# Performance work log

Measured on AMD Instinct MI355X. Metric: run time of the kernel, lower is better.

Reference implementation:

```python
import jax, jax.numpy as jnp
import numpy as np

N, E, F, R, L, B = 50000, 800000, 64, 20, 2, 64
RC = 5.0
ZMAX = 100
LN2 = 0.6931471805599453

def ssp(x):
    # shifted softplus: softplus(x) - log(2)
    return jax.nn.softplus(x) - LN2

def setup_inputs() -> dict:
    key = jax.random.key(0)
    ks = jax.random.split(key, 32)
    w = lambda i, shape: jax.random.normal(ks[i], shape, dtype=jnp.float32) * 0.05
    inp = {
        'z': jax.random.randint(ks[0], (N,), 0, ZMAX + 1),
        'pos': jax.random.normal(ks[1], (N, 3), dtype=jnp.float32) * 3.0,
        'edge_index': jax.random.randint(ks[2], (2, E), 0, N),
        'batch_idx': jnp.sort(jax.random.randint(ks[3], (N,), 0, B)),
        'emb': jax.random.normal(ks[4], (ZMAX + 1, F), dtype=jnp.float32),
        'phi_W': w(5, (L, 3 * F, F)), 'phi_b': w(6, (L, 3 * F)),
        'filt_W1': w(7, (L, F, R)), 'filt_b1': w(8, (L, F)),
        'filt_W2': w(9, (L, 3 * F, F)), 'filt_b2': w(10, (L, 3 * F)),
        'U_W': w(11, (L, F, F)), 'V_W': w(12, (L, F, F)),
        'a_W1': w(13, (L, F, 2 * F)), 'a_b1': w(14, (L, F)),
        'a_W2': w(15, (L, 3 * F, F)), 'a_b2': w(16, (L, 3 * F)),
        'e_W1': w(17, (F // 2, F)), 'e_b1': w(18, (F // 2,)),
        'e_W2': w(19, (1, F // 2)), 'e_b2': w(20, (1,)),
        'dip_w': w(21, (F,)),
    }
    return inp

def reference(z, pos, edge_index, batch_idx, emb, phi_W, phi_b,
              filt_W1, filt_b1, filt_W2, filt_b2, U_W, V_W,
              a_W1, a_b1, a_W2, a_b2, e_W1, e_b1, e_W2, e_b2, dip_w):
    src, dst = edge_index[0], edge_index[1]
    s = emb[z]                               # (N, F)
    v = jnp.zeros((N, F, 3), dtype=s.dtype)  # (N, F, 3)

    # edge geometry
    r_vec = pos[dst] - pos[src]              # (E, 3)
    r_norm = jnp.linalg.norm(r_vec, axis=-1)
    r_hat = r_vec / jnp.maximum(r_norm, 1e-8)[:, None]
    # Gaussian RBF on [0, RC], widths = grid spacing
    mu = jnp.linspace(0.0, RC, R, dtype=s.dtype)
    width = mu[1] - mu[0]
    e_ij = jnp.exp(-((r_norm[:, None] - mu[None, :]) ** 2) / (2.0 * width * width))
    fc = 0.5 * (jnp.cos(jnp.pi * r_norm / RC) + 1.0) * (r_norm < RC)
    e_ij = e_ij * fc[:, None]                # (E, R)

    for l in range(L):
        # message block
        filt = ssp(e_ij @ filt_W1[l].T + filt_b1[l]) @ filt_W2[l].T + filt_b2[l]  # (E, 3F)
        W_s, W_v, W_r = jnp.split(filt, 3, axis=-1)
        phi = s[dst] @ phi_W[l].T + phi_b[l]                                       # (E, 3F)
        phi_s, phi_v, phi_r = jnp.split(phi, 3, axis=-1)
        m_s = W_s * phi_s                                                          # (E, F)
        m_v = W_v[:, :, None] * v[dst] + (W_r * phi_r)[:, :, None] * r_hat[:, None, :]  # (E, F, 3)
        s = s + jax.ops.segment_sum(m_s, src, num_segments=N)
        v = v + jax.ops.segment_sum(m_v, src, num_segments=N)
        # update block
        Uv = jnp.einsum('nfd,gf->ngd', v, U_W[l])
        Vv = jnp.einsum('nfd,gf->ngd', v, V_W[l])
        Vv_norm_sq = jnp.sum(Vv * Vv, axis=-1)                                     # (N, F)
        a = ssp(jnp.concatenate([s, Vv_norm_sq], axis=-1) @ a_W1[l].T + a_b1[l]) @ a_W2[l].T + a_b2[l]
        a_ss, a_sv, a_vv = jnp.split(a, 3, axis=-1)
        inner = jnp.sum(Uv * Vv, axis=-1)
        s = s + a_ss + a_sv * inner
        v = v + a_vv[:, :, None] * Uv

    # heads
    eps_i = (ssp(s @ e_W1.T + e_b1) @ e_W2.T + e_b2)[:, 0]  # (N,)
    energy = jax.ops.segment_sum(eps_i, batch_idx, num_segments=B)
    mu_i = jnp.sum(v * dip_w[None, :, None], axis=1)         # (N, 3)
    mu_mol = jax.ops.segment_sum(mu_i, batch_idx, num_segments=B)
    dipole = jnp.linalg.norm(mu_mol, axis=-1)
    charges = jnp.zeros((N,), dtype=s.dtype)
    return energy, dipole, charges
```

## Files before the change

kernel.cpp:

```cpp
#include <hip/hip_runtime.h>
#include <math.h>

static constexpr int N  = 50000;
static constexpr int E  = 800000;
static constexpr int F  = 64;
static constexpr int R  = 20;
static constexpr int NL = 2;
static constexpr int B  = 64;
static constexpr float RC   = 5.0f;
static constexpr float LN2F = 0.6931471805599453f;
static constexpr float WIDTH  = RC / (R - 1);
static constexpr float INV2W2 = 1.0f / (2.0f * WIDTH * WIDTH);
static constexpr float PI_F = 3.14159265358979323846f;

static constexpr int   NB     = 4096;
static constexpr float DR     = RC / NB;
static constexpr float INV_DR = NB / RC;
static constexpr int   TROWS  = NB + 2;
static constexpr int   TENT   = NB + 1;

static constexpr int NBLK_SCAN = (N + 255) / 256;

typedef __attribute__((ext_vector_type(8))) short bf16x8;
typedef __attribute__((ext_vector_type(4))) float f32x4;

__device__ __forceinline__ float ssp_f(float x) {
    return fmaxf(x, 0.0f) + log1pf(__expf(-fabsf(x))) - LN2F;
}

__device__ __forceinline__ short f2bf(float x) {
    unsigned u = __builtin_bit_cast(unsigned, x);
    unsigned r = (u + 0x7fffu + ((u >> 16) & 1u)) >> 16;
    return (short)r;
}
__device__ __forceinline__ float bf_lo(unsigned u) {
    return __builtin_bit_cast(float, u << 16);
}
__device__ __forceinline__ float bf_hi(unsigned u) {
    return __builtin_bit_cast(float, u & 0xffff0000u);
}

__global__ void k_hist(const int* __restrict__ ei, int* __restrict__ cnt) {
    int e = blockIdx.x * blockDim.x + threadIdx.x;
    if (e < E) atomicAdd(&cnt[ei[e]], 1);
}

__global__ void k_scan_a(const int* __restrict__ cnt, int* __restrict__ bsum) {
    __shared__ int part[256];
    const int t = threadIdx.x;
    const int idx = blockIdx.x * 256 + t;
    int v = (idx < N) ? cnt[idx] : 0;
    part[t] = v;
    __syncthreads();
    for (int d = 1; d < 256; d <<= 1) {
        int x = (t >= d) ? part[t - d] : 0;
        __syncthreads();
        part[t] += x;
        __syncthreads();
    }
    if (t == 255) bsum[blockIdx.x] = part[255];
}

__global__ void k_scan_b(const int* __restrict__ bsum, int* __restrict__ bpre,
                         int* __restrict__ offN) {
    __shared__ int part[256];
    const int t = threadIdx.x;
    int v = (t < NBLK_SCAN) ? bsum[t] : 0;
    part[t] = v;
    __syncthreads();
    for (int d = 1; d < 256; d <<= 1) {
        int x = (t >= d) ? part[t - d] : 0;
        __syncthreads();
        part[t] += x;
        __syncthreads();
    }
    if (t < NBLK_SCAN) bpre[t] = part[t] - v;
    if (t == NBLK_SCAN - 1) *offN = part[t];
}

__global__ void k_scan_c(const int* __restrict__ cnt, const int* __restrict__ bpre,
                         int* __restrict__ off, int* __restrict__ cur) {
    __shared__ int part[256];
    const int t = threadIdx.x;
    const int idx = blockIdx.x * 256 + t;
    int v = (idx < N) ? cnt[idx] : 0;
    part[t] = v;
    __syncthreads();
    for (int d = 1; d < 256; d <<= 1) {
        int x = (t >= d) ? part[t - d] : 0;
        __syncthreads();
        part[t] += x;
        __syncthreads();
    }
    if (idx < N) {
        int e = bpre[blockIdx.x] + part[t] - v;
        off[idx] = e;
        cur[idx] = e;
    }
}

__global__ void k_scatter(const int* __restrict__ ei, int* __restrict__ cur,
                          const float* __restrict__ pos, uint4* __restrict__ edata) {
    int e = blockIdx.x * blockDim.x + threadIdx.x;
    if (e >= E) return;
    int src = ei[e], dst = ei[E + e];
    int p = atomicAdd(&cur[src], 1);
    float qx = pos[dst * 3 + 0] - pos[src * 3 + 0];
    float qy = pos[dst * 3 + 1] - pos[src * 3 + 1];
    float qz = pos[dst * 3 + 2] - pos[src * 3 + 2];
    float rn = sqrtf(qx * qx + qy * qy + qz * qz);
    float invn = 1.0f / fmaxf(rn, 1e-8f);
    float t = rn * INV_DR;
    int i = (int)t;
    float fr = t - (float)i;
    if (i >= NB) { i = NB; fr = 0.0f; }
    uint4 rec;
    rec.x = (unsigned)dst;
    rec.y = (unsigned)i | ((unsigned)(unsigned short)f2bf(fr) << 16);
    rec.z = (unsigned)(unsigned short)f2bf(qx * invn)
          | ((unsigned)(unsigned short)f2bf(qy * invn) << 16);
    rec.w = (unsigned)(unsigned short)f2bf(qz * invn);
    edata[p] = rec;
}

__global__ void k_table(const float* __restrict__ fW1, const float* __restrict__ fb1,
                        const float* __restrict__ fW2, const float* __restrict__ fb2,
                        unsigned short* __restrict__ Tp) {
    const int l   = blockIdx.x / TROWS;
    const int row = blockIdx.x % TROWS;
    const int lane = threadIdx.x;
    const float r = fminf((float)row, (float)NB) * DR;
    const float fc = (r < RC) ? 0.5f * (__cosf(PI_F * r * (1.0f / RC)) + 1.0f) : 0.0f;

    __shared__ float sh[F];
    float acc = fb1[l * F + lane];
    const float* w1 = fW1 + (size_t)l * F * R + (size_t)lane * R;
    #pragma unroll
    for (int rr = 0; rr < R; rr++) {
        float dmu = r - rr * WIDTH;
        float er = __expf(-dmu * dmu * INV2W2) * fc;
        acc = fmaf(er, w1[rr], acc);
    }
    sh[lane] = ssp_f(acc);
    __syncthreads();
    unsigned short* TpL = Tp + (size_t)l * TENT * 512;
    #pragma unroll
    for (int p = 0; p < 3; p++) {
        int c = p * 64 + lane;
        float a = fb2[l * 192 + c];
        const float* w2 = fW2 + ((size_t)l * 192 + c) * 64;
        #pragma unroll 8
        for (int k = 0; k < F; k++) a = fmaf(sh[k], w2[k], a);
        unsigned short bf = (unsigned short)f2bf(a);
        if (row <= NB) TpL[(size_t)row * 512 + lane * 8 + p * 2 + 0] = bf;
        if (row >= 1)  TpL[(size_t)(row - 1) * 512 + lane * 8 + p * 2 + 1] = bf;
    }
    if (row <= NB) {
        TpL[(size_t)row * 512 + lane * 8 + 6] = 0;
        TpL[(size_t)row * 512 + lane * 8 + 7] = 0;
    }
}

__launch_bounds__(256)
__global__ void k_pack0(float* __restrict__ s, const int* __restrict__ z,
                        const float* __restrict__ emb,
                        const float* __restrict__ PW, const float* __restrict__ Pb,
                        unsigned* __restrict__ ndA) {
    __shared__ float sbuf[4][F];
    const int lane = threadIdx.x & 63;
    const int wid  = threadIdx.x >> 6;
    const int gwave = blockIdx.x * 4 + wid;
    const int nwaves = gridDim.x * 4;

    float wsr[F], wrr[F];
    {
        const float* rs = PW + (size_t)lane * 64;
        const float* rr = PW + (size_t)(128 + lane) * 64;
        #pragma unroll
        for (int k = 0; k < F; k += 4) {
            float4 a = *(const float4*)(rs + k);
            wsr[k] = a.x; wsr[k+1] = a.y; wsr[k+2] = a.z; wsr[k+3] = a.w;
            float4 b = *(const float4*)(rr + k);
            wrr[k] = b.x; wrr[k+1] = b.y; wrr[k+2] = b.z; wrr[k+3] = b.w;
        }
    }
    const float bs = Pb[lane], br = Pb[128 + lane];

    for (int n = gwave; n < N; n += nwaves) {
        float sv = emb[(size_t)z[n] * F + lane];
        s[(size_t)n * F + lane] = sv;
        sbuf[wid][lane] = sv;
        float as = bs, ar = br;
        #pragma unroll
        for (int k = 0; k < F; k += 4) {
            float4 s4 = *(const float4*)&sbuf[wid][k];
            as = fmaf(s4.x, wsr[k],   as); as = fmaf(s4.y, wsr[k+1], as);
            as = fmaf(s4.z, wsr[k+2], as); as = fmaf(s4.w, wsr[k+3], as);
            ar = fmaf(s4.x, wrr[k],   ar); ar = fmaf(s4.y, wrr[k+1], ar);
            ar = fmaf(s4.z, wrr[k+2], ar); ar = fmaf(s4.w, wrr[k+3], ar);
        }
        ndA[(size_t)n * 64 + lane] = (unsigned)(unsigned short)f2bf(as)
                                   | ((unsigned)(unsigned short)f2bf(ar) << 16);
    }
}

template<bool ACCUMV>
__device__ __forceinline__ void edge_step(const uint4 ed,
                                          const unsigned short* __restrict__ TpL,
                                          const unsigned* __restrict__ ndA,
                                          const uint2* __restrict__ ndV, int lane,
                                          float& ms, float& mv0, float& mv1, float& mv2) {
    const int   i  = (int)(ed.y & 0xffffu);
    const float fr = bf_hi(ed.y);
    const uint4 t  = *(const uint4*)(TpL + (size_t)i * 512 + lane * 8);
    const unsigned a = ndA[(size_t)ed.x * 64 + lane];
    const float Ws = fmaf(fr, bf_hi(t.x) - bf_lo(t.x), bf_lo(t.x));
    const float Wr = fmaf(fr, bf_hi(t.z) - bf_lo(t.z), bf_lo(t.z));
    ms = fmaf(Ws, bf_lo(a), ms);
    const float c = Wr * bf_hi(a);
    const float rhx = bf_lo(ed.z), rhy = bf_hi(ed.z), rhz = bf_lo(ed.w);
    if (ACCUMV) {
        const float Wv = fmaf(fr, bf_hi(t.y) - bf_lo(t.y), bf_lo(t.y));
        const uint2 w = ndV[(size_t)ed.x * 64 + lane];
        mv0 = fmaf(Wv, bf_lo(w.x), fmaf(c, rhx, mv0));
        mv1 = fmaf(Wv, bf_hi(w.x), fmaf(c, rhy, mv1));
        mv2 = fmaf(Wv, bf_lo(w.y), fmaf(c, rhz, mv2));
    } else {
        mv0 = fmaf(c, rhx, mv0);
        mv1 = fmaf(c, rhy, mv1);
        mv2 = fmaf(c, rhz, mv2);
    }
}

template<bool ACCUMV>
__launch_bounds__(256, 1)
__global__ void k_gather(const uint4* __restrict__ edata, const int* __restrict__ off,
                         const unsigned short* __restrict__ TpL,
                         const unsigned* __restrict__ ndA, const uint2* __restrict__ ndV,
                         float* __restrict__ s, float* __restrict__ v) {
    __shared__ float red[4][4][64];
    const int lane = threadIdx.x & 63;
    const int wv   = threadIdx.x >> 6;
    const int n = blockIdx.x;
    const int base = off[n], end = off[n + 1];

    float ms = 0.f, mv0 = 0.f, mv1 = 0.f, mv2 = 0.f;
    int k = base + wv;
    if (k < end) {
        uint4 ed = edata[k];
        for (;;) {
            const int kn = k + 4;
            const bool more = kn < end;
            uint4 edn;
            if (more) edn = edata[kn];
            edge_step<ACCUMV>(ed, TpL, ndA, ndV, lane, ms, mv0, mv1, mv2);
            if (!more) break;
            ed = edn;
            k = kn;
        }
    }
    red[wv][0][lane] = ms;
    red[wv][1][lane] = mv0;
    red[wv][2][lane] = mv1;
    red[wv][3][lane] = mv2;
    __syncthreads();
    if (wv == 0) {
        ms  = red[0][0][lane] + red[1][0][lane] + red[2][0][lane] + red[3][0][lane];
        mv0 = red[0][1][lane] + red[1][1][lane] + red[2][1][lane] + red[3][1][lane];
        mv1 = red[0][2][lane] + red[1][2][lane] + red[2][2][lane] + red[3][2][lane];
        mv2 = red[0][3][lane] + red[1][3][lane] + red[2][3][lane] + red[3][3][lane];
        s[(size_t)n * F + lane] += ms;
        float* vo = v + (size_t)n * 3 * F + lane;
        if (ACCUMV) {
            vo[0]     += mv0;
            vo[F]     += mv1;
            vo[2 * F] += mv2;
        } else {
            vo[0] = mv0; vo[F] = mv1; vo[2 * F] = mv2;
        }
    }
}

__device__ __forceinline__ bf16x8 load_wfrag(const float* __restrict__ Wp, int ldk,
                                             int nrow, int k0) {
    const float* p = Wp + (size_t)nrow * ldk + k0;
    float4 a = *(const float4*)p;
    float4 b = *(const float4*)(p + 4);
    bf16x8 r;
    r[0] = f2bf(a.x); r[1] = f2bf(a.y); r[2] = f2bf(a.z); r[3] = f2bf(a.w);
    r[4] = f2bf(b.x); r[5] = f2bf(b.y); r[6] = f2bf(b.z); r[7] = f2bf(b.w);
    return r;
}

template<bool DO_PACK>
__launch_bounds__(256)
__global__ void k_update_mfma(float* __restrict__ s, float* __restrict__ v,
                              const float* __restrict__ U_W, const float* __restrict__ V_W,
                              const float* __restrict__ aW1, const float* __restrict__ ab1,
                              const float* __restrict__ aW2, const float* __restrict__ ab2,
                              const float* __restrict__ PW, const float* __restrict__ Pb,
                              unsigned* __restrict__ ndA, uint2* __restrict__ ndV) {
    __shared__ short vlds[96 * 72];
    __shared__ short xlds[32 * 136];
    __shared__ short hlds[32 * 72];

    const int tid = threadIdx.x;
    const int l   = tid & 63;
    const int w   = tid >> 6;
    const int lo  = l & 15;
    const int hi  = l >> 4;

    bf16x8 ufr[2], vfr[2], w1fr[4], w2fr[3][2];
    #pragma unroll
    for (int kk = 0; kk < 2; kk++) {
        ufr[kk] = load_wfrag(U_W, 64, w * 16 + lo, kk * 32 + hi * 8);
        vfr[kk] = load_wfrag(V_W, 64, w * 16 + lo, kk * 32 + hi * 8);
    }
    #pragma unroll
    for (int kk = 0; kk < 4; kk++)
        w1fr[kk] = load_wfrag(aW1, 128, w * 16 + lo, kk * 32 + hi * 8);
    #pragma unroll
    for (int p = 0; p < 3; p++)
        #pragma unroll
        for (int kk = 0; kk < 2; kk++)
            w2fr[p][kk] = load_wfrag(aW2, 64, p * 64 + w * 16 + lo, kk * 32 + hi * 8);

    bf16x8 pws[2], pwr[2];
    float pbs = 0.f, pbr = 0.f;
    if (DO_PACK) {
        #pragma unroll
        for (int kk = 0; kk < 2; kk++) {
            pws[kk] = load_wfrag(PW, 64, w * 16 + lo, kk * 32 + hi * 8);
            pwr[kk] = load_wfrag(PW, 64, 128 + w * 16 + lo, kk * 32 + hi * 8);
        }
        pbs = Pb[w * 16 + lo];
        pbr = Pb[128 + w * 16 + lo];
    }

    const float ab1c  = ab1[w * 16 + lo];
    const float ab2c0 = ab2[w * 16 + lo];
    const float ab2c1 = ab2[64 + w * 16 + lo];
    const float ab2c2 = ab2[128 + w * 16 + lo];
    const int g = w * 16 + lo;

    for (int half = 0; half < 2; half++) {
        const int n0 = blockIdx.x * 64 + half * 32;
        if (half) __syncthreads();

        for (int u = tid; u < 96 * 8; u += 256) {
            int row = u >> 3, oct = u & 7;
            int d = row >> 5, nn = row & 31;
            int n = min(n0 + nn, N - 1);
            const float* src = v + ((size_t)n * 3 + d) * 64 + oct * 8;
            float4 a = *(const float4*)src;
            float4 b = *(const float4*)(src + 4);
            bf16x8 t;
            t[0] = f2bf(a.x); t[1] = f2bf(a.y); t[2] = f2bf(a.z); t[3] = f2bf(a.w);
            t[4] = f2bf(b.x); t[5] = f2bf(b.y); t[6] = f2bf(b.z); t[7] = f2bf(b.w);
            *(bf16x8*)&vlds[row * 72 + oct * 8] = t;
        }
        for (int u = tid; u < 32 * 8; u += 256) {
            int nn = u >> 3, oct = u & 7;
            int n = min(n0 + nn, N - 1);
            const float* src = s + (size_t)n * 64 + oct * 8;
            float4 a = *(const float4*)src;
            float4 b = *(const float4*)(src + 4);
            bf16x8 t;
            t[0] = f2bf(a.x); t[1] = f2bf(a.y); t[2] = f2bf(a.z); t[3] = f2bf(a.w);
            t[4] = f2bf(b.x); t[5] = f2bf(b.y); t[6] = f2bf(b.z); t[7] = f2bf(b.w);
            *(bf16x8*)&xlds[nn * 136 + oct * 8] = t;
        }
        __syncthreads();

        f32x4 cu[6], cv[6];
        #pragma unroll
        for (int mt = 0; mt < 6; mt++) { cu[mt] = (f32x4)0.0f; cv[mt] = (f32x4)0.0f; }
        #pragma unroll
        for (int kk = 0; kk < 2; kk++) {
            #pragma unroll
            for (int mt = 0; mt < 6; mt++) {
                bf16x8 af = *(const bf16x8*)&vlds[(mt * 16 + lo) * 72 + kk * 32 + hi * 8];
                cu[mt] = __builtin_amdgcn_mfma_f32_16x16x32_bf16(af, ufr[kk], cu[mt], 0, 0, 0);
                cv[mt] = __builtin_amdgcn_mfma_f32_16x16x32_bf16(af, vfr[kk], cv[mt], 0, 0, 0);
            }
        }

        f32x4 inn[2];
        #pragma unroll
        for (int nt = 0; nt < 2; nt++) {
            #pragma unroll
            for (int r = 0; r < 4; r++) {
                float vs = 0.f, ii = 0.f;
                #pragma unroll
                for (int d = 0; d < 3; d++) {
                    float a = cu[d * 2 + nt][r], b = cv[d * 2 + nt][r];
                    vs = fmaf(b, b, vs);
                    ii = fmaf(a, b, ii);
                }
                inn[nt][r] = ii;
                int nl = nt * 16 + hi * 4 + r;
                xlds[nl * 136 + 64 + w * 16 + lo] = f2bf(vs);
            }
        }
        __syncthreads();

        f32x4 c2[2];
        c2[0] = (f32x4)0.0f; c2[1] = (f32x4)0.0f;
        #pragma unroll
        for (int kk = 0; kk < 4; kk++) {
            #pragma unroll
            for (int mt = 0; mt < 2; mt++) {
                bf16x8 af = *(const bf16x8*)&xlds[(mt * 16 + lo) * 136 + kk * 32 + hi * 8];
                c2[mt] = __builtin_amdgcn_mfma_f32_16x16x32_bf16(af, w1fr[kk], c2[mt], 0, 0, 0);
            }
        }
        #pragma unroll
        for (int mt = 0; mt < 2; mt++)
            #pragma unroll
            for (int r = 0; r < 4; r++) {
                float hv = ssp_f(c2[mt][r] + ab1c);
                hlds[(mt * 16 + hi * 4 + r) * 72 + w * 16 + lo] = f2bf(hv);
            }
        __syncthreads();

        f32x4 c3[2][3];
        #pragma unroll
        for (int mt = 0; mt < 2; mt++)
            #pragma unroll
            for (int p = 0; p < 3; p++) c3[mt][p] = (f32x4)0.0f;
        #pragma unroll
        for (int kk = 0; kk < 2; kk++) {
            #pragma unroll
            for (int mt = 0; mt < 2; mt++) {
                bf16x8 af = *(const bf16x8*)&hlds[(mt * 16 + lo) * 72 + kk * 32 + hi * 8];
                #pragma unroll
                for (int p = 0; p < 3; p++)
                    c3[mt][p] = __builtin_amdgcn_mfma_f32_16x16x32_bf16(af, w2fr[p][kk], c3[mt][p], 0, 0, 0);
            }
        }

        float snew[2][4];
        #pragma unroll
        for (int mt = 0; mt < 2; mt++) {
            #pragma unroll
            for (int r = 0; r < 4; r++) {
                int n = n0 + mt * 16 + hi * 4 + r;
                if (n >= N) { snew[mt][r] = 0.f; continue; }
                float a_ss = c3[mt][0][r] + ab2c0;
                float a_sv = c3[mt][1][r] + ab2c1;
                float a_vv = c3[mt][2][r] + ab2c2;
                size_t si = (size_t)n * 64 + g;
                float sn = s[si] + a_ss + a_sv * inn[mt][r];
                s[si] = sn;
                snew[mt][r] = sn;
                float vn[3];
                #pragma unroll
                for (int d = 0; d < 3; d++) {
                    size_t vi = ((size_t)n * 3 + d) * 64 + g;
                    vn[d] = v[vi] + a_vv * cu[d * 2 + mt][r];
                    v[vi] = vn[d];
                }
                if (DO_PACK) {
                    uint2 pv;
                    pv.x = (unsigned)(unsigned short)f2bf(vn[0])
                         | ((unsigned)(unsigned short)f2bf(vn[1]) << 16);
                    pv.y = (unsigned)(unsigned short)f2bf(vn[2]);
                    ndV[(size_t)n * 64 + g] = pv;
                }
            }
        }

        if (DO_PACK) {
            __syncthreads();
            #pragma unroll
            for (int mt = 0; mt < 2; mt++)
                #pragma unroll
                for (int r = 0; r < 4; r++)
                    hlds[(mt * 16 + hi * 4 + r) * 72 + g] = f2bf(snew[mt][r]);
            __syncthreads();

            f32x4 cs[2], cr[2];
            cs[0] = (f32x4)0.0f; cs[1] = (f32x4)0.0f;
            cr[0] = (f32x4)0.0f; cr[1] = (f32x4)0.0f;
            #pragma unroll
            for (int kk = 0; kk < 2; kk++) {
                #pragma unroll
                for (int mt = 0; mt < 2; mt++) {
                    bf16x8 af = *(const bf16x8*)&hlds[(mt * 16 + lo) * 72 + kk * 32 + hi * 8];
                    cs[mt] = __builtin_amdgcn_mfma_f32_16x16x32_bf16(af, pws[kk], cs[mt], 0, 0, 0);
                    cr[mt] = __builtin_amdgcn_mfma_f32_16x16x32_bf16(af, pwr[kk], cr[mt], 0, 0, 0);
                }
            }
            #pragma unroll
            for (int mt = 0; mt < 2; mt++) {
                #pragma unroll
                for (int r = 0; r < 4; r++) {
                    int n = n0 + mt * 16 + hi * 4 + r;
                    if (n >= N) continue;
                    ndA[(size_t)n * 64 + g] =
                          (unsigned)(unsigned short)f2bf(cs[mt][r] + pbs)
                        | ((unsigned)(unsigned short)f2bf(cr[mt][r] + pbr) << 16);
                }
            }
        }
    }
}

__global__ void k_heads(const float* __restrict__ s, const float* __restrict__ v,
                        const int* __restrict__ batch_idx,
                        const float* __restrict__ eW1, const float* __restrict__ eb1,
                        const float* __restrict__ eW2, const float* __restrict__ eb2,
                        const float* __restrict__ dip_w,
                        float* __restrict__ eacc, float* __restrict__ macc) {
    __shared__ float se[B];
    __shared__ float sm[3][B];
    if (threadIdx.x < B) se[threadIdx.x] = 0.0f;
    if (threadIdx.x < 3 * B) sm[threadIdx.x >> 6][threadIdx.x & 63] = 0.0f;
    __syncthreads();
    int n = blockIdx.x * blockDim.x + threadIdx.x;
    if (n < N) {
        int b = batch_idx[n];
        float sr[F];
        #pragma unroll
        for (int f = 0; f < F; f += 4) {
            float4 t = *(const float4*)&s[(size_t)n * F + f];
            sr[f] = t.x; sr[f+1] = t.y; sr[f+2] = t.z; sr[f+3] = t.w;
        }
        float eps = eb2[0];
        for (int jj = 0; jj < F / 2; jj++) {
            float acc = eb1[jj];
            #pragma unroll
            for (int f = 0; f < F; f++)
                acc = fmaf(sr[f], eW1[jj * F + f], acc);
            eps = fmaf(eW2[jj], ssp_f(acc), eps);
        }
        atomicAdd(&se[b], eps);
        #pragma unroll
        for (int d = 0; d < 3; d++) {
            float m = 0.0f;
            #pragma unroll 8
            for (int f = 0; f < F; f++)
                m = fmaf(v[((size_t)n * 3 + d) * F + f], dip_w[f], m);
            atomicAdd(&sm[d][b], m);
        }
    }
    __syncthreads();
    if (threadIdx.x < B) atomicAdd(&eacc[threadIdx.x], se[threadIdx.x]);
    if (threadIdx.x >= B && threadIdx.x < 4 * B) {
        int d = (threadIdx.x >> 6) - 1, b = threadIdx.x & 63;
        atomicAdd(&macc[d * B + b], sm[d][b]);
    }
}

__global__ void k_final(const float* __restrict__ eacc, const float* __restrict__ macc,
                        float* __restrict__ out) {
    int b = threadIdx.x;
    if (b < B) {
        out[b] = eacc[b];
        float mx = macc[b], my = macc[B + b], mz = macc[2 * B + b];
        out[B + b] = sqrtf(mx * mx + my * my + mz * mz);
    }
}

extern "C" void kernel_launch(void* const* d_in, const int* in_sizes, int n_in,
                              void* d_out, int out_size, void* d_ws, size_t ws_size,
                              hipStream_t stream) {
    const int*   z     = (const int*)d_in[0];
    const float* pos   = (const float*)d_in[1];
    const int*   ei    = (const int*)d_in[2];
    const int*   bidx  = (const int*)d_in[3];
    const float* emb   = (const float*)d_in[4];
    const float* phi_W = (const float*)d_in[5];
    const float* phi_b = (const float*)d_in[6];
    const float* fW1   = (const float*)d_in[7];
    const float* fb1   = (const float*)d_in[8];
    const float* fW2   = (const float*)d_in[9];
    const float* fb2   = (const float*)d_in[10];
    const float* U_W   = (const float*)d_in[11];
    const float* V_W   = (const float*)d_in[12];
    const float* aW1   = (const float*)d_in[13];
    const float* ab1   = (const float*)d_in[14];
    const float* aW2   = (const float*)d_in[15];
    const float* ab2   = (const float*)d_in[16];
    const float* eW1   = (const float*)d_in[17];
    const float* eb1   = (const float*)d_in[18];
    const float* eW2   = (const float*)d_in[19];
    const float* eb2   = (const float*)d_in[20];
    const float* dip_w = (const float*)d_in[21];
    float* out = (float*)d_out;

    float* ws = (float*)d_ws;
    float* s    = ws;
    float* v    = s + (size_t)N * F;
    unsigned* ndA = (unsigned*)(v + (size_t)N * F * 3);
    uint2* ndV  = (uint2*)(ndA + (size_t)N * 64);
    unsigned short* Tp = (unsigned short*)(ndV + (size_t)N * 64);
    float* eacc = (float*)(Tp + (size_t)NL * TENT * 512);
    float* macc = eacc + B;
    int*   cnt  = (int*)(macc + 3 * B);
    int*   off  = cnt  + N;
    int*   cur  = off  + N + 1;
    int*   bsum = cur  + N;
    int*   bpre = bsum + 256;
    uint4* edata = (uint4*)(((uintptr_t)(bpre + 256) + 15) & ~(uintptr_t)15);

    hipMemsetAsync(cnt,  0, sizeof(int) * N, stream);
    hipMemsetAsync(eacc, 0, sizeof(float) * 4 * B, stream);
    hipMemsetAsync(out + 2 * B, 0, sizeof(float) * (size_t)N, stream);

    k_hist<<<(E + 255) / 256, 256, 0, stream>>>(ei, cnt);
    k_scan_a<<<NBLK_SCAN, 256, 0, stream>>>(cnt, bsum);
    k_scan_b<<<1, 256, 0, stream>>>(bsum, bpre, off + N);
    k_scan_c<<<NBLK_SCAN, 256, 0, stream>>>(cnt, bpre, off, cur);
    k_scatter<<<(E + 255) / 256, 256, 0, stream>>>(ei, cur, pos, edata);
    k_table<<<NL * TROWS, 64, 0, stream>>>(fW1, fb1, fW2, fb2, Tp);

    const int ublocks = (N + 63) / 64;
    k_pack0<<<512, 256, 0, stream>>>(s, z, emb, phi_W, phi_b, ndA);
    k_gather<false><<<N, 256, 0, stream>>>(edata, off, Tp, ndA, ndV, s, v);
    k_update_mfma<true><<<ublocks, 256, 0, stream>>>(s, v,
        U_W, V_W, aW1, ab1, aW2, ab2,
        phi_W + (size_t)192 * 64, phi_b + 192, ndA, ndV);
    k_gather<true><<<N, 256, 0, stream>>>(edata, off,
        Tp + (size_t)TENT * 512, ndA, ndV, s, v);
    k_update_mfma<false><<<ublocks, 256, 0, stream>>>(s, v,
        U_W + 4096, V_W + 4096, aW1 + 8192, ab1 + F, aW2 + 12288, ab2 + 192,
        nullptr, nullptr, nullptr, nullptr);

    k_heads<<<(N + 255) / 256, 256, 0, stream>>>(s, v, bidx, eW1, eb1, eW2, eb2,
                                                 dip_w, eacc, macc);
    k_final<<<1, 64, 0, stream>>>(eacc, macc, out);
}
```

Baseline: 555.4 us.

## Interleave node records, shrink filter table rows, deepen gather prefetch

Merges the separate per-node scalar and vector bf16 records into one interleaved 12-byte record per (node, feature), so each edge needs one gather instead of two. It also shrinks the filter lookup table from 16 to 12 bytes per lane by dropping padding. The gather loop now software-pipelines the table and node-record loads one edge ahead, and the launch bound is raised to allow 8 blocks per CU. The risks are 12-byte (3-dword) vector loads that may not coalesce as well as aligned 8- or 16-byte ones, and higher register pressure from the deeper prefetch.

Measured after the change: 540.7 us. -2.6%, faster.

```diff
diff --git a/kernel.cpp b/kernel.cpp
--- a/kernel.cpp
+++ b/kernel.cpp
@@ -23,6 +23,7 @@
 
 typedef __attribute__((ext_vector_type(8))) short bf16x8;
 typedef __attribute__((ext_vector_type(4))) float f32x4;
+typedef __attribute__((ext_vector_type(3))) unsigned uint32x3;
 
 __device__ __forceinline__ float ssp_f(float x) {
     return fmaxf(x, 0.0f) + log1pf(__expf(-fabsf(x))) - LN2F;
@@ -143,7 +144,7 @@
     }
     sh[lane] = ssp_f(acc);
     __syncthreads();
-    unsigned short* TpL = Tp + (size_t)l * TENT * 512;
+    unsigned short* TpL = Tp + (size_t)l * TENT * 384;
     #pragma unroll
     for (int p = 0; p < 3; p++) {
         int c = p * 64 + lane;
@@ -152,12 +153,8 @@
         #pragma unroll 8
         for (int k = 0; k < F; k++) a = fmaf(sh[k], w2[k], a);
         unsigned short bf = (unsigned short)f2bf(a);
-        if (row <= NB) TpL[(size_t)row * 512 + lane * 8 + p * 2 + 0] = bf;
-        if (row >= 1)  TpL[(size_t)(row - 1) * 512 + lane * 8 + p * 2 + 1] = bf;
-    }
-    if (row <= NB) {
-        TpL[(size_t)row * 512 + lane * 8 + 6] = 0;
-        TpL[(size_t)row * 512 + lane * 8 + 7] = 0;
+        if (row <= NB) TpL[(size_t)row * 384 + lane * 6 + p * 2 + 0] = bf;
+        if (row >= 1)  TpL[(size_t)(row - 1) * 384 + lane * 6 + p * 2 + 1] = bf;
     }
 }
 
@@ -165,7 +162,7 @@
 __global__ void k_pack0(float* __restrict__ s, const int* __restrict__ z,
                         const float* __restrict__ emb,
                         const float* __restrict__ PW, const float* __restrict__ Pb,
-                        unsigned* __restrict__ ndA) {
+                        unsigned* __restrict__ ndAV) {
     __shared__ float sbuf[4][F];
     const int lane = threadIdx.x & 63;
     const int wid  = threadIdx.x >> 6;
@@ -199,32 +196,46 @@
             ar = fmaf(s4.x, wrr[k],   ar); ar = fmaf(s4.y, wrr[k+1], ar);
             ar = fmaf(s4.z, wrr[k+2], ar); ar = fmaf(s4.w, wrr[k+3], ar);
         }
-        ndA[(size_t)n * 64 + lane] = (unsigned)(unsigned short)f2bf(as)
-                                   | ((unsigned)(unsigned short)f2bf(ar) << 16);
-    }
+        ndAV[((size_t)n * 64 + lane) * 3] =
+              (unsigned)(unsigned short)f2bf(as)
+            | ((unsigned)(unsigned short)f2bf(ar) << 16);
+    }
+}
+
+__device__ __forceinline__ uint32x3 load_tbl(const unsigned short* __restrict__ TpL,
+                                             unsigned edy, int lane) {
+    const int i = (int)(edy & 0xffffu);
+    return *(const uint32x3*)(TpL + (size_t)i * 384 + lane * 6);
 }
 
 template<bool ACCUMV>
-__device__ __forceinline__ void edge_step(const uint4 ed,
-                                          const unsigned short* __restrict__ TpL,
-                                          const unsigned* __restrict__ ndA,
-                                          const uint2* __restrict__ ndV, int lane,
-                                          float& ms, float& mv0, float& mv1, float& mv2) {
-    const int   i  = (int)(ed.y & 0xffffu);
+__device__ __forceinline__ uint32x3 load_rec(const unsigned* __restrict__ ndAV,
+                                             unsigned dst, int lane) {
+    const unsigned* p = ndAV + ((size_t)dst * 64 + lane) * 3;
+    uint32x3 r;
+    if (ACCUMV) {
+        r = *(const uint32x3*)p;
+    } else {
+        r.x = *p; r.y = 0; r.z = 0;
+    }
+    return r;
+}
+
+template<bool ACCUMV>
+__device__ __forceinline__ void consume_edge(const uint4 ed, const uint32x3 t,
+                                             const uint32x3 r,
+                                             float& ms, float& mv0, float& mv1, float& mv2) {
     const float fr = bf_hi(ed.y);
-    const uint4 t  = *(const uint4*)(TpL + (size_t)i * 512 + lane * 8);
-    const unsigned a = ndA[(size_t)ed.x * 64 + lane];
     const float Ws = fmaf(fr, bf_hi(t.x) - bf_lo(t.x), bf_lo(t.x));
     const float Wr = fmaf(fr, bf_hi(t.z) - bf_lo(t.z), bf_lo(t.z));
-    ms = fmaf(Ws, bf_lo(a), ms);
-    const float c = Wr * bf_hi(a);
+    ms = fmaf(Ws, bf_lo(r.x), ms);
+    const float c = Wr * bf_hi(r.x);
     const float rhx = bf_lo(ed.z), rhy = bf_hi(ed.z), rhz = bf_lo(ed.w);
     if (ACCUMV) {
         const float Wv = fmaf(fr, bf_hi(t.y) - bf_lo(t.y), bf_lo(t.y));
-        const uint2 w = ndV[(size_t)ed.x * 64 + lane];
-        mv0 = fmaf(Wv, bf_lo(w.x), fmaf(c, rhx, mv0));
-        mv1 = fmaf(Wv, bf_hi(w.x), fmaf(c, rhy, mv1));
-        mv2 = fmaf(Wv, bf_lo(w.y), fmaf(c, rhz, mv2));
+        mv0 = fmaf(Wv, bf_lo(r.y), fmaf(c, rhx, mv0));
+        mv1 = fmaf(Wv, bf_hi(r.y), fmaf(c, rhy, mv1));
+        mv2 = fmaf(Wv, bf_lo(r.z), fmaf(c, rhz, mv2));
     } else {
         mv0 = fmaf(c, rhx, mv0);
         mv1 = fmaf(c, rhy, mv1);
@@ -233,10 +244,10 @@
 }
 
 template<bool ACCUMV>
-__launch_bounds__(256, 1)
+__launch_bounds__(256, 8)
 __global__ void k_gather(const uint4* __restrict__ edata, const int* __restrict__ off,
                          const unsigned short* __restrict__ TpL,
-                         const unsigned* __restrict__ ndA, const uint2* __restrict__ ndV,
+                         const unsigned* __restrict__ ndAV,
                          float* __restrict__ s, float* __restrict__ v) {
     __shared__ float red[4][4][64];
     const int lane = threadIdx.x & 63;
@@ -245,18 +256,29 @@
     const int base = off[n], end = off[n + 1];
 
     float ms = 0.f, mv0 = 0.f, mv1 = 0.f, mv2 = 0.f;
-    int k = base + wv;
-    if (k < end) {
-        uint4 ed = edata[k];
+    int kc = base + wv;
+    if (kc < end) {
+        uint4 edC = edata[kc];
+        int kn = kc + 4;
+        bool hasN = kn < end;
+        uint4 edN = edC;
+        if (hasN) edN = edata[kn];
+        uint32x3 tC = load_tbl(TpL, edC.y, lane);
+        uint32x3 rC = load_rec<ACCUMV>(ndAV, edC.x, lane);
         for (;;) {
-            const int kn = k + 4;
-            const bool more = kn < end;
-            uint4 edn;
-            if (more) edn = edata[kn];
-            edge_step<ACCUMV>(ed, TpL, ndA, ndV, lane, ms, mv0, mv1, mv2);
-            if (!more) break;
-            ed = edn;
-            k = kn;
+            const int kn2 = kn + 4;
+            const bool hasN2 = hasN && (kn2 < end);
+            uint4 edN2 = edC;
+            if (hasN2) edN2 = edata[kn2];
+            uint32x3 tN = tC, rN = rC;
+            if (hasN) {
+                tN = load_tbl(TpL, edN.y, lane);
+                rN = load_rec<ACCUMV>(ndAV, edN.x, lane);
+            }
+            consume_edge<ACCUMV>(edC, tC, rC, ms, mv0, mv1, mv2);
+            if (!hasN) break;
+            edC = edN; tC = tN; rC = rN;
+            edN = edN2; hasN = hasN2; kn = kn2;
         }
     }
     red[wv][0][lane] = ms;
@@ -299,7 +321,7 @@
                               const float* __restrict__ aW1, const float* __restrict__ ab1,
                               const float* __restrict__ aW2, const float* __restrict__ ab2,
                               const float* __restrict__ PW, const float* __restrict__ Pb,
-                              unsigned* __restrict__ ndA, uint2* __restrict__ ndV) {
+                              unsigned* __restrict__ ndAV) {
     __shared__ short vlds[96 * 72];
     __shared__ short xlds[32 * 136];
     __shared__ short hlds[32 * 72];
@@ -461,11 +483,10 @@
                     v[vi] = vn[d];
                 }
                 if (DO_PACK) {
-                    uint2 pv;
-                    pv.x = (unsigned)(unsigned short)f2bf(vn[0])
-                         | ((unsigned)(unsigned short)f2bf(vn[1]) << 16);
-                    pv.y = (unsigned)(unsigned short)f2bf(vn[2]);
-                    ndV[(size_t)n * 64 + g] = pv;
+                    unsigned* pp = ndAV + ((size_t)n * 64 + g) * 3;
+                    pp[1] = (unsigned)(unsigned short)f2bf(vn[0])
+                          | ((unsigned)(unsigned short)f2bf(vn[1]) << 16);
+                    pp[2] = (unsigned)(unsigned short)f2bf(vn[2]);
                 }
             }
         }
@@ -497,7 +518,7 @@
                 for (int r = 0; r < 4; r++) {
                     int n = n0 + mt * 16 + hi * 4 + r;
                     if (n >= N) continue;
-                    ndA[(size_t)n * 64 + g] =
+                    ndAV[((size_t)n * 64 + g) * 3] =
                           (unsigned)(unsigned short)f2bf(cs[mt][r] + pbs)
                         | ((unsigned)(unsigned short)f2bf(cr[mt][r] + pbr) << 16);
                 }
@@ -592,10 +613,9 @@
     float* ws = (float*)d_ws;
     float* s    = ws;
     float* v    = s + (size_t)N * F;
-    unsigned* ndA = (unsigned*)(v + (size_t)N * F * 3);
-    uint2* ndV  = (uint2*)(ndA + (size_t)N * 64);
-    unsigned short* Tp = (unsigned short*)(ndV + (size_t)N * 64);
-    float* eacc = (float*)(Tp + (size_t)NL * TENT * 512);
+    unsigned* ndAV = (unsigned*)(v + (size_t)N * F * 3);
+    unsigned short* Tp = (unsigned short*)(ndAV + (size_t)N * 64 * 3);
+    float* eacc = (float*)(Tp + (size_t)NL * TENT * 384);
     float* macc = eacc + B;
     int*   cnt  = (int*)(macc + 3 * B);
     int*   off  = cnt  + N;
@@ -616,16 +636,16 @@
     k_table<<<NL * TROWS, 64, 0, stream>>>(fW1, fb1, fW2, fb2, Tp);
 
     const int ublocks = (N + 63) / 64;
-    k_pack0<<<512, 256, 0, stream>>>(s, z, emb, phi_W, phi_b, ndA);
-    k_gather<false><<<N, 256, 0, stream>>>(edata, off, Tp, ndA, ndV, s, v);
+    k_pack0<<<512, 256, 0, stream>>>(s, z, emb, phi_W, phi_b, ndAV);
+    k_gather<false><<<N, 256, 0, stream>>>(edata, off, Tp, ndAV, s, v);
     k_update_mfma<true><<<ublocks, 256, 0, stream>>>(s, v,
         U_W, V_W, aW1, ab1, aW2, ab2,
-        phi_W + (size_t)192 * 64, phi_b + 192, ndA, ndV);
+        phi_W + (size_t)192 * 64, phi_b + 192, ndAV);
     k_gather<true><<<N, 256, 0, stream>>>(edata, off,
-        Tp + (size_t)TENT * 512, ndA, ndV, s, v);
+        Tp + (size_t)TENT * 384, ndAV, s, v);
     k_update_mfma<false><<<ublocks, 256, 0, stream>>>(s, v,
         U_W + 4096, V_W + 4096, aW1 + 8192, ab1 + F, aW2 + 12288, ab2 + 192,
-        nullptr, nullptr, nullptr, nullptr);
+        nullptr, nullptr, nullptr);
 
     k_heads<<<(N + 255) / 256, 256, 0, stream>>>(s, v, bidx, eW1, eb1, eW2, eb2,
                                                  dip_w, eacc, macc);
```

## Partition edges into near/far ranges and specialize far-edge gather loop

Applied to the files above, without the earlier changes.

The scatter step now fills each node's edge list from both ends: in-cutoff edges grow forward and edges beyond the cutoff grow backward. A mid pointer separates the two ranges. The gather kernel handles far edges with a constant filter row loaded once, so those edges skip the per-edge table lookup and interpolation, and their node loads are software-pipelined. The filter table is packed tighter (6 bf16 per lane instead of 8), and launch bounds now allow more blocks per CU, which trades fewer registers for higher occupancy. Edges within one node are now reordered, so the floating-point summation order changes.

Result: faster. 527.9 us (-4.9%).

```diff
diff --git a/kernel.cpp b/kernel.cpp
--- a/kernel.cpp
+++ b/kernel.cpp
@@ -23,6 +23,7 @@
 
 typedef __attribute__((ext_vector_type(8))) short bf16x8;
 typedef __attribute__((ext_vector_type(4))) float f32x4;
+typedef __attribute__((ext_vector_type(3))) unsigned uint32x3;
 
 __device__ __forceinline__ float ssp_f(float x) {
     return fmaxf(x, 0.0f) + log1pf(__expf(-fabsf(x))) - LN2F;
@@ -79,7 +80,8 @@
 }
 
 __global__ void k_scan_c(const int* __restrict__ cnt, const int* __restrict__ bpre,
-                         int* __restrict__ off, int* __restrict__ cur) {
+                         int* __restrict__ off, int* __restrict__ curN,
+                         int* __restrict__ curF) {
     __shared__ int part[256];
     const int t = threadIdx.x;
     const int idx = blockIdx.x * 256 + t;
@@ -95,16 +97,17 @@
     if (idx < N) {
         int e = bpre[blockIdx.x] + part[t] - v;
         off[idx] = e;
-        cur[idx] = e;
-    }
-}
-
-__global__ void k_scatter(const int* __restrict__ ei, int* __restrict__ cur,
+        curN[idx] = e;
+        curF[idx] = e + v;
+    }
+}
+
+__global__ void k_scatter(const int* __restrict__ ei, int* __restrict__ curN,
+                          int* __restrict__ curF,
                           const float* __restrict__ pos, uint4* __restrict__ edata) {
     int e = blockIdx.x * blockDim.x + threadIdx.x;
     if (e >= E) return;
     int src = ei[e], dst = ei[E + e];
-    int p = atomicAdd(&cur[src], 1);
     float qx = pos[dst * 3 + 0] - pos[src * 3 + 0];
     float qy = pos[dst * 3 + 1] - pos[src * 3 + 1];
     float qz = pos[dst * 3 + 2] - pos[src * 3 + 2];
@@ -113,7 +116,9 @@
     float t = rn * INV_DR;
     int i = (int)t;
     float fr = t - (float)i;
-    if (i >= NB) { i = NB; fr = 0.0f; }
+    const bool far = (i >= NB);
+    if (far) { i = NB; fr = 0.0f; }
+    int p = far ? (atomicAdd(&curF[src], -1) - 1) : atomicAdd(&curN[src], 1);
     uint4 rec;
     rec.x = (unsigned)dst;
     rec.y = (unsigned)i | ((unsigned)(unsigned short)f2bf(fr) << 16);
@@ -143,7 +148,7 @@
     }
     sh[lane] = ssp_f(acc);
     __syncthreads();
-    unsigned short* TpL = Tp + (size_t)l * TENT * 512;
+    unsigned short* TpL = Tp + (size_t)l * TENT * 384;
     #pragma unroll
     for (int p = 0; p < 3; p++) {
         int c = p * 64 + lane;
@@ -152,12 +157,8 @@
         #pragma unroll 8
         for (int k = 0; k < F; k++) a = fmaf(sh[k], w2[k], a);
         unsigned short bf = (unsigned short)f2bf(a);
-        if (row <= NB) TpL[(size_t)row * 512 + lane * 8 + p * 2 + 0] = bf;
-        if (row >= 1)  TpL[(size_t)(row - 1) * 512 + lane * 8 + p * 2 + 1] = bf;
-    }
-    if (row <= NB) {
-        TpL[(size_t)row * 512 + lane * 8 + 6] = 0;
-        TpL[(size_t)row * 512 + lane * 8 + 7] = 0;
+        if (row <= NB) TpL[(size_t)row * 384 + lane * 6 + p * 2 + 0] = bf;
+        if (row >= 1)  TpL[(size_t)(row - 1) * 384 + lane * 6 + p * 2 + 1] = bf;
     }
 }
 
@@ -205,36 +206,9 @@
 }
 
 template<bool ACCUMV>
-__device__ __forceinline__ void edge_step(const uint4 ed,
-                                          const unsigned short* __restrict__ TpL,
-                                          const unsigned* __restrict__ ndA,
-                                          const uint2* __restrict__ ndV, int lane,
-                                          float& ms, float& mv0, float& mv1, float& mv2) {
-    const int   i  = (int)(ed.y & 0xffffu);
-    const float fr = bf_hi(ed.y);
-    const uint4 t  = *(const uint4*)(TpL + (size_t)i * 512 + lane * 8);
-    const unsigned a = ndA[(size_t)ed.x * 64 + lane];
-    const float Ws = fmaf(fr, bf_hi(t.x) - bf_lo(t.x), bf_lo(t.x));
-    const float Wr = fmaf(fr, bf_hi(t.z) - bf_lo(t.z), bf_lo(t.z));
-    ms = fmaf(Ws, bf_lo(a), ms);
-    const float c = Wr * bf_hi(a);
-    const float rhx = bf_lo(ed.z), rhy = bf_hi(ed.z), rhz = bf_lo(ed.w);
-    if (ACCUMV) {
-        const float Wv = fmaf(fr, bf_hi(t.y) - bf_lo(t.y), bf_lo(t.y));
-        const uint2 w = ndV[(size_t)ed.x * 64 + lane];
-        mv0 = fmaf(Wv, bf_lo(w.x), fmaf(c, rhx, mv0));
-        mv1 = fmaf(Wv, bf_hi(w.x), fmaf(c, rhy, mv1));
-        mv2 = fmaf(Wv, bf_lo(w.y), fmaf(c, rhz, mv2));
-    } else {
-        mv0 = fmaf(c, rhx, mv0);
-        mv1 = fmaf(c, rhy, mv1);
-        mv2 = fmaf(c, rhz, mv2);
-    }
-}
-
-template<bool ACCUMV>
-__launch_bounds__(256, 1)
+__launch_bounds__(256, 8)
 __global__ void k_gather(const uint4* __restrict__ edata, const int* __restrict__ off,
+                         const int* __restrict__ mid,
                          const unsigned short* __restrict__ TpL,
                          const unsigned* __restrict__ ndA, const uint2* __restrict__ ndV,
                          float* __restrict__ s, float* __restrict__ v) {
@@ -242,23 +216,77 @@
     const int lane = threadIdx.x & 63;
     const int wv   = threadIdx.x >> 6;
     const int n = blockIdx.x;
-    const int base = off[n], end = off[n + 1];
+    const int base = off[n], m = mid[n], end = off[n + 1];
 
     float ms = 0.f, mv0 = 0.f, mv1 = 0.f, mv2 = 0.f;
-    int k = base + wv;
-    if (k < end) {
-        uint4 ed = edata[k];
-        for (;;) {
-            const int kn = k + 4;
-            const bool more = kn < end;
-            uint4 edn;
-            if (more) edn = edata[kn];
-            edge_step<ACCUMV>(ed, TpL, ndA, ndV, lane, ms, mv0, mv1, mv2);
-            if (!more) break;
-            ed = edn;
-            k = kn;
-        }
-    }
+
+    for (int k = base + wv; k < m; k += 4) {
+        const uint4 ed = edata[k];
+        const int i = (int)(ed.y & 0xffffu);
+        const uint32x3 t = *(const uint32x3*)(TpL + (size_t)i * 384 + lane * 6);
+        const unsigned a = ndA[(size_t)ed.x * 64 + lane];
+        const float fr = bf_hi(ed.y);
+        const float Ws = fmaf(fr, bf_hi(t.x) - bf_lo(t.x), bf_lo(t.x));
+        const float Wr = fmaf(fr, bf_hi(t.z) - bf_lo(t.z), bf_lo(t.z));
+        ms = fmaf(Ws, bf_lo(a), ms);
+        const float c = Wr * bf_hi(a);
+        const float rhx = bf_lo(ed.z), rhy = bf_hi(ed.z), rhz = bf_lo(ed.w);
+        if (ACCUMV) {
+            const float Wv = fmaf(fr, bf_hi(t.y) - bf_lo(t.y), bf_lo(t.y));
+            const uint2 w = ndV[(size_t)ed.x * 64 + lane];
+            mv0 = fmaf(Wv, bf_lo(w.x), fmaf(c, rhx, mv0));
+            mv1 = fmaf(Wv, bf_hi(w.x), fmaf(c, rhy, mv1));
+            mv2 = fmaf(Wv, bf_lo(w.y), fmaf(c, rhz, mv2));
+        } else {
+            mv0 = fmaf(c, rhx, mv0);
+            mv1 = fmaf(c, rhy, mv1);
+            mv2 = fmaf(c, rhz, mv2);
+        }
+    }
+
+    {
+        const uint32x3 tF = *(const uint32x3*)(TpL + (size_t)NB * 384 + lane * 6);
+        const float WsF = bf_lo(tF.x), WvF = bf_lo(tF.y), WrF = bf_lo(tF.z);
+        int kc = m + wv;
+        if (kc < end) {
+            uint4 edC = edata[kc];
+            int kn = kc + 4;
+            bool hasN = kn < end;
+            uint4 edN = edC;
+            if (hasN) edN = edata[kn];
+            unsigned aC = ndA[(size_t)edC.x * 64 + lane];
+            uint2 wC = {0, 0};
+            if (ACCUMV) wC = ndV[(size_t)edC.x * 64 + lane];
+            for (;;) {
+                const int kn2 = kn + 4;
+                const bool hasN2 = hasN && (kn2 < end);
+                uint4 edN2 = edC;
+                if (hasN2) edN2 = edata[kn2];
+                unsigned aN = aC;
+                uint2 wN = wC;
+                if (hasN) {
+                    aN = ndA[(size_t)edN.x * 64 + lane];
+                    if (ACCUMV) wN = ndV[(size_t)edN.x * 64 + lane];
+                }
+                ms = fmaf(WsF, bf_lo(aC), ms);
+                const float c = WrF * bf_hi(aC);
+                const float rhx = bf_lo(edC.z), rhy = bf_hi(edC.z), rhz = bf_lo(edC.w);
+                if (ACCUMV) {
+                    mv0 = fmaf(WvF, bf_lo(wC.x), fmaf(c, rhx, mv0));
+                    mv1 = fmaf(WvF, bf_hi(wC.x), fmaf(c, rhy, mv1));
+                    mv2 = fmaf(WvF, bf_lo(wC.y), fmaf(c, rhz, mv2));
+                } else {
+                    mv0 = fmaf(c, rhx, mv0);
+                    mv1 = fmaf(c, rhy, mv1);
+                    mv2 = fmaf(c, rhz, mv2);
+                }
+                if (!hasN) break;
+                edC = edN; aC = aN; wC = wN;
+                edN = edN2; hasN = hasN2; kn = kn2;
+            }
+        }
+    }
+
     red[wv][0][lane] = ms;
     red[wv][1][lane] = mv0;
     red[wv][2][lane] = mv1;
@@ -595,12 +623,13 @@
     unsigned* ndA = (unsigned*)(v + (size_t)N * F * 3);
     uint2* ndV  = (uint2*)(ndA + (size_t)N * 64);
     unsigned short* Tp = (unsigned short*)(ndV + (size_t)N * 64);
-    float* eacc = (float*)(Tp + (size_t)NL * TENT * 512);
+    float* eacc = (float*)(Tp + (size_t)NL * TENT * 384);
     float* macc = eacc + B;
     int*   cnt  = (int*)(macc + 3 * B);
     int*   off  = cnt  + N;
-    int*   cur  = off  + N + 1;
-    int*   bsum = cur  + N;
+    int*   curN = off  + N + 1;
+    int*   curF = curN + N;
+    int*   bsum = curF + N;
     int*   bpre = bsum + 256;
     uint4* edata = (uint4*)(((uintptr_t)(bpre + 256) + 15) & ~(uintptr_t)15);
 
@@ -611,18 +640,18 @@
     k_hist<<<(E + 255) / 256, 256, 0, stream>>>(ei, cnt);
     k_scan_a<<<NBLK_SCAN, 256, 0, stream>>>(cnt, bsum);
     k_scan_b<<<1, 256, 0, stream>>>(bsum, bpre, off + N);
-    k_scan_c<<<NBLK_SCAN, 256, 0, stream>>>(cnt, bpre, off, cur);
-    k_scatter<<<(E + 255) / 256, 256, 0, stream>>>(ei, cur, pos, edata);
+    k_scan_c<<<NBLK_SCAN, 256, 0, stream>>>(cnt, bpre, off, curN, curF);
+    k_scatter<<<(E + 255) / 256, 256, 0, stream>>>(ei, curN, curF, pos, edata);
     k_table<<<NL * TROWS, 64, 0, stream>>>(fW1, fb1, fW2, fb2, Tp);
 
     const int ublocks = (N + 63) / 64;
     k_pack0<<<512, 256, 0, stream>>>(s, z, emb, phi_W, phi_b, ndA);
-    k_gather<false><<<N, 256, 0, stream>>>(edata, off, Tp, ndA, ndV, s, v);
+    k_gather<false><<<N, 256, 0, stream>>>(edata, off, curN, Tp, ndA, ndV, s, v);
     k_update_mfma<true><<<ublocks, 256, 0, stream>>>(s, v,
         U_W, V_W, aW1, ab1, aW2, ab2,
         phi_W + (size_t)192 * 64, phi_b + 192, ndA, ndV);
-    k_gather<true><<<N, 256, 0, stream>>>(edata, off,
-        Tp + (size_t)TENT * 512, ndA, ndV, s, v);
+    k_gather<true><<<N, 256, 0, stream>>>(edata, off, curN,
+        Tp + (size_t)TENT * 384, ndA, ndV, s, v);
     k_update_mfma<false><<<ublocks, 256, 0, stream>>>(s, v,
         U_W + 4096, V_W + 4096, aW1 + 8192, ab1 + F, aW2 + 12288, ab2 + 192,
         nullptr, nullptr, nullptr, nullptr);
```
